# Optimization experiments

Hardware: AMD Instinct MI355X
Metric: run time of the kernel (lower is better)

## Reference

```python
import jax, jax.numpy as jnp
import numpy as np

STRIDE = 32
NUM_CLASSES = 20
CONF_THRESH = 0.01
NMS_THRESH = 0.5
INPUT_H, INPUT_W = 1024, 1024
EPS = 1e-28


def make_grid(h, w):
    hs, ws = h // STRIDE, w // STRIDE
    gy, gx = jnp.meshgrid(jnp.arange(hs), jnp.arange(ws), indexing='ij')
    # [1, hs*ws, 2] (x, y) cell coordinates
    return jnp.stack([gx, gy], axis=-1).reshape(1, hs * ws, 2).astype(jnp.float32)


def decode_boxes(txtytwth, grid):
    # txtytwth: [B, N, 4] -> [xmin, ymin, xmax, ymax] in pixels
    cxy = (jax.nn.sigmoid(txtytwth[..., :2]) + grid) * STRIDE
    wh = jnp.exp(txtytwth[..., 2:])
    return jnp.concatenate([cxy - wh * 0.5, cxy + wh * 0.5], axis=-1)


def pairwise_iou(boxes):
    # boxes: [N, 4]; faithful to source: area without +1, w/h clamped to 1e-28
    x1, y1, x2, y2 = boxes[:, 0], boxes[:, 1], boxes[:, 2], boxes[:, 3]
    areas = (x2 - x1) * (y2 - y1)
    xx1 = jnp.maximum(x1[:, None], x1[None, :])
    yy1 = jnp.maximum(y1[:, None], y1[None, :])
    xx2 = jnp.minimum(x2[:, None], x2[None, :])
    yy2 = jnp.minimum(y2[:, None], y2[None, :])
    w = jnp.maximum(EPS, xx2 - xx1)
    h = jnp.maximum(EPS, yy2 - yy1)
    inter = w * h
    return inter / (areas[:, None] + areas[None, :] - inter)


def nms_single(boxes, scores, valid):
    # greedy NMS, fixed-shape: returns keep mask [N] in original order
    n = boxes.shape[0]
    order = jnp.argsort(-scores)
    b = boxes[order]
    v = valid[order]
    iou = pairwise_iou(b)  # [N, N]
    idx = jnp.arange(n)

    def body(i, keep):
        sup = keep[i] & (iou[i] > NMS_THRESH) & (idx > i)
        return keep & jnp.logical_not(sup)

    keep_sorted = jax.lax.fori_loop(0, n, body, v)
    return jnp.zeros(n, dtype=bool).at[order].set(keep_sorted)


def setup_inputs() -> dict:
    key = jax.random.key(0)
    k1, k2, k3 = jax.random.split(key, 3)
    feat = jax.random.normal(k1, (64, 512, 32, 32), dtype=jnp.float32)
    w_pred = jax.random.normal(k2, (25, 512), dtype=jnp.float32) * 0.05
    b_pred = jax.random.normal(k3, (25,), dtype=jnp.float32) * 0.05
    return {"feat": feat, "w_pred": w_pred, "b_pred": b_pred}


def reference(feat, w_pred, b_pred):
    B, C, hs, ws = feat.shape
    N = hs * ws
    # 1x1 conv head: [B, 25, hs, ws] -> [B, N, 25]
    pred = jnp.einsum('bchw,oc->bhwo', feat, w_pred) + b_pred
    pred = pred.reshape(B, N, 1 + NUM_CLASSES + 4)

    conf = jax.nn.sigmoid(pred[..., :1])                      # [B, N, 1]
    cls = jax.nn.softmax(pred[..., 1:1 + NUM_CLASSES], -1)    # [B, N, 20]
    boxes = decode_boxes(pred[..., 1 + NUM_CLASSES:], make_grid(INPUT_H, INPUT_W))
    scale = jnp.array([INPUT_W, INPUT_H, INPUT_W, INPUT_H], jnp.float32)
    boxes = jnp.clip(boxes / scale, 0.0, 1.0)                 # [B, N, 4] in [0,1]

    scores_all = conf * cls                                   # [B, N, 20]
    cls_inds = jnp.argmax(scores_all, axis=-1)                # [B, N]
    scores = jnp.max(scores_all, axis=-1)                     # [B, N]
    valid = scores > CONF_THRESH

    # class-aware NMS via per-class coordinate offset (boxes in [0,1])
    off_boxes = boxes + cls_inds[..., None].astype(jnp.float32) * 2.0
    keep = jax.vmap(nms_single)(off_boxes, scores, valid)     # [B, N] bool
    return boxes, scores, cls_inds.astype(jnp.int32), keep
```

## Files before the change

### kernel.cpp

```cpp
#include <hip/hip_runtime.h>
#include <hip/hip_bf16.h>

typedef unsigned long long u64;
typedef unsigned int u32;
typedef __attribute__((ext_vector_type(4))) double f64x4;

#define NB   64
#define NPOS 1024
#define NOUT 25
#define NCLS 20
#define WROW 32
#define BIGCAP 256
#define ECAP   2048
#define TINY_TH (30.0f / 1024.0f)

#define OFF_W64   0
#define OFF_B64   131072
#define OFF_BIGC  131328
#define OFF_BIGL  131584
#define OFF_EDGC  197120
#define OFF_EDGL  197376

__global__ __launch_bounds__(256) void k_cvt(const float* __restrict__ w,
                                             const float* __restrict__ bias,
                                             double* __restrict__ wpad,
                                             double* __restrict__ b64,
                                             int* __restrict__ bigcnt,
                                             int* __restrict__ edgecnt)
{
    int idx = blockIdx.x * 256 + threadIdx.x;
    if (idx < 512 * WROW) {
        int c = idx >> 5, o = idx & 31;
        wpad[idx] = (o < NOUT) ? (double)w[o * 512 + c] : 0.0;
    }
    if (idx < NOUT) b64[idx] = (double)bias[idx];
    if (idx < NB) { bigcnt[idx] = 0; edgecnt[idx] = 0; }
}

__device__ __forceinline__ void epilogue(const double* __restrict__ acc,
                                         const double* __restrict__ b64,
                                         int b, int n,
                                         float* __restrict__ boxes_out,
                                         float* __restrict__ scores_out,
                                         float* __restrict__ cls_out,
                                         int* __restrict__ bigcnt,
                                         int* __restrict__ biglist)
{
    double p[NOUT];
#pragma unroll
    for (int o = 0; o < NOUT; ++o) p[o] = acc[o] + b64[o];

    double conf = 1.0 / (1.0 + exp(-p[0]));
    double m = p[1]; int ci = 0;
#pragma unroll
    for (int i = 2; i <= NCLS; ++i) {
        if (p[i] > m) { m = p[i]; ci = i - 1; }
    }
    double ssum = 0.0;
#pragma unroll
    for (int i = 0; i < NCLS; ++i) ssum += exp(p[1 + i] - m);
    double best = conf / ssum;

    int gx = n & 31, gy = n >> 5;
    double sx = 1.0 / (1.0 + exp(-p[21]));
    double sy = 1.0 / (1.0 + exp(-p[22]));
    double cx = (sx + (double)gx) * 32.0;
    double cy = (sy + (double)gy) * 32.0;
    double bw = exp(p[23]), bh = exp(p[24]);
    double x1 = (cx - bw * 0.5) * (1.0 / 1024.0);
    double y1 = (cy - bh * 0.5) * (1.0 / 1024.0);
    double x2 = (cx + bw * 0.5) * (1.0 / 1024.0);
    double y2 = (cy + bh * 0.5) * (1.0 / 1024.0);
    x1 = fmin(fmax(x1, 0.0), 1.0); y1 = fmin(fmax(y1, 0.0), 1.0);
    x2 = fmin(fmax(x2, 0.0), 1.0); y2 = fmin(fmax(y2, 0.0), 1.0);

    float fx1 = (float)x1, fy1 = (float)y1, fx2 = (float)x2, fy2 = (float)y2;
    int gi = b * NPOS + n;
    ((float4*)boxes_out)[gi] = make_float4(fx1, fy1, fx2, fy2);
    scores_out[gi] = (float)best;
    cls_out[gi]    = (float)ci;

    if (!((fx2 - fx1 < TINY_TH) && (fy2 - fy1 < TINY_TH))) {
        int s = atomicAdd(&bigcnt[b], 1);
        if (s < BIGCAP) biglist[b * BIGCAP + s] = n;
    }
}

__global__ __launch_bounds__(256, 4) void k_main(const float* __restrict__ feat,
                                                 const double* __restrict__ wpad_g,
                                                 const double* __restrict__ b64,
                                                 float* __restrict__ boxes_out,
                                                 float* __restrict__ scores_out,
                                                 float* __restrict__ cls_out,
                                                 int* __restrict__ bigcnt,
                                                 int* __restrict__ biglist)
{
    __shared__ __align__(16) char smem[32768];
    float*  AbF = (float*)smem;
    double* BbF = (double*)(smem + 16384);
    double (*pd)[33] = (double(*)[33])smem;

    const int b   = blockIdx.y;
    const int tid = threadIdx.x;
    const int l   = tid & 63;
    const int wv  = tid >> 6;
    const int pg  = wv >> 1;
    const int oh  = wv & 1;
    const int n0  = blockIdx.x * 64;

    double ca = ((l >> 4) == 0) ? (double)(l & 15) : 0.0;
    double cb = ((l >> 4) == 0) ? 1.0 : 0.0;
    f64x4 cd = {0.0, 0.0, 0.0, 0.0};
    cd = __builtin_amdgcn_mfma_f64_16x16x4f64(ca, cb, cd, 0, 0, 0);
    int rmap[4];
#pragma unroll
    for (int v = 0; v < 4; ++v) {
        int r = (int)(cd[v] + 0.5);
        rmap[v] = (r < 0) ? 0 : (r > 15 ? 15 : r);
    }

    const float* __restrict__ featb = feat + (size_t)b * 512 * NPOS + n0;

#define A_SRC(C0, IT) (((const float4*)(featb + (size_t)((C0) + wv*8 + (IT)*4 + (l>>4)) * NPOS)) + (l & 15))
#define B_SRC(C0, IT) (((const double2*)(wpad_g + (size_t)((C0) + wv*8 + (IT)*4 + (l>>4)) * WROW)) + (l & 15))
#define A_DST(BUF, IT) ((float4*)(AbF + (BUF)*2048 + (wv*8 + (IT)*4) * 64 + l*4))
#define B_DST(BUF, IT) ((double2*)(BbF + (BUF)*1024 + (wv*8 + (IT)*4) * 32 + l*2))

    f64x4 acc0 = {0.0, 0.0, 0.0, 0.0};
    f64x4 acc1 = {0.0, 0.0, 0.0, 0.0};

    float4  ra0 = *A_SRC(0, 0), ra1 = *A_SRC(0, 1);
    double2 rb0 = *B_SRC(0, 0), rb1 = *B_SRC(0, 1);
    *A_DST(0, 0) = ra0;  *A_DST(0, 1) = ra1;
    *B_DST(0, 0) = rb0;  *B_DST(0, 1) = rb1;
    __syncthreads();

#pragma unroll 1
    for (int t = 0; t < 16; ++t) {
        const int buf = t & 1;
        const bool more = (t + 1) < 16;
        const int c1 = (t + 1) * 32;
        if (more) {
            ra0 = *A_SRC(c1, 0);  ra1 = *A_SRC(c1, 1);
            rb0 = *B_SRC(c1, 0);  rb1 = *B_SRC(c1, 1);
        }
#pragma unroll
        for (int s = 0; s < 8; ++s) {
            const int rowA = buf*2048 + (4*s + (l >> 4)) * 64 + pg * 32 + (l & 15);
            const int rowB = buf*1024 + (4*s + (l >> 4)) * 32 + oh * 16 + (l & 15);
            double av0 = (double)AbF[rowA];
            double av1 = (double)AbF[rowA + 16];
            double bv  = BbF[rowB];
            acc0 = __builtin_amdgcn_mfma_f64_16x16x4f64(av0, bv, acc0, 0, 0, 0);
            acc1 = __builtin_amdgcn_mfma_f64_16x16x4f64(av1, bv, acc1, 0, 0, 0);
        }
        if (more) {
            *A_DST(buf ^ 1, 0) = ra0;  *A_DST(buf ^ 1, 1) = ra1;
            *B_DST(buf ^ 1, 0) = rb0;  *B_DST(buf ^ 1, 1) = rb1;
        }
        __syncthreads();
    }
#undef A_SRC
#undef B_SRC
#undef A_DST
#undef B_DST

#pragma unroll
    for (int v = 0; v < 4; ++v) {
        int r0 = pg * 32 + rmap[v];
        pd[r0][oh * 16 + (l & 15)]      = acc0[v];
        pd[r0 + 16][oh * 16 + (l & 15)] = acc1[v];
    }
    __syncthreads();

    if (tid < 64) {
        double acc[NOUT];
#pragma unroll
        for (int o = 0; o < NOUT; ++o) acc[o] = pd[tid][o];
        int n = n0 + tid;
        epilogue(acc, b64, b, n, boxes_out, scores_out, cls_out, bigcnt, biglist);
    }
}

__device__ __forceinline__ void pair_check(int b, int p, int i,
                                           float4 bp, float ap, int cp,
                                           const float4* __restrict__ boxes4,
                                           const float* __restrict__ scores,
                                           const float* __restrict__ cls,
                                           int* __restrict__ edgecnt,
                                           u32* __restrict__ edges,
                                           bool need_tiny_i)
{
    float si = scores[b * NPOS + i];
    if (si <= 0.01f) return;
    float4 bi = boxes4[b * NPOS + i];
    if (need_tiny_i) {
        if (!((bi.z - bi.x < TINY_TH) && (bi.w - bi.y < TINY_TH))) return;
    }
    if ((int)cls[b * NPOS + i] != cp) return;
    float xx1 = fmaxf(bi.x, bp.x), yy1 = fmaxf(bi.y, bp.y);
    float xx2 = fminf(bi.z, bp.z), yy2 = fminf(bi.w, bp.w);
    float ww = fmaxf(1e-28f, xx2 - xx1);
    float hh = fmaxf(1e-28f, yy2 - yy1);
    float inter = ww * hh;
    float ai = (bi.z - bi.x) * (bi.w - bi.y);
    float uni = ai + ap - inter;
    if (uni > 0.0f && inter > 0.5f * uni) {
        int u = p < i ? p : i, v = p < i ? i : p;
        int slot = atomicAdd(&edgecnt[b], 1);
        if (slot < ECAP) edges[(size_t)b * ECAP + slot] = ((u32)u << 16) | (u32)v;
    }
}

__global__ __launch_bounds__(256) void k_edge(const float4* __restrict__ boxes4,
                                              const float* __restrict__ scores,
                                              const float* __restrict__ cls,
                                              const int* __restrict__ bigcnt,
                                              const int* __restrict__ biglist,
                                              int* __restrict__ edgecnt,
                                              u32* __restrict__ edges)
{
    const int b = blockIdx.y;
    const int p = blockIdx.x * 256 + threadIdx.x;
    const float sp = scores[b * NPOS + p];
    if (sp <= 0.01f) return;
    const float4 bp = boxes4[b * NPOS + p];
    const float ap = (bp.z - bp.x) * (bp.w - bp.y);
    const int cp = (int)cls[b * NPOS + p];
    const bool tinyp = (bp.z - bp.x < TINY_TH) && (bp.w - bp.y < TINY_TH);
    const int gx = p & 31, gy = p >> 5;

    if (tinyp) {
        if (gy > 0 && gx > 0)  pair_check(b, p, p - 33, bp, ap, cp, boxes4, scores, cls, edgecnt, edges, true);
        if (gy > 0)            pair_check(b, p, p - 32, bp, ap, cp, boxes4, scores, cls, edgecnt, edges, true);
        if (gy > 0 && gx < 31) pair_check(b, p, p - 31, bp, ap, cp, boxes4, scores, cls, edgecnt, edges, true);
        if (gx > 0)            pair_check(b, p, p - 1,  bp, ap, cp, boxes4, scores, cls, edgecnt, edges, true);
    }
    int nb = bigcnt[b]; if (nb > BIGCAP) nb = BIGCAP;
    for (int t = 0; t < nb; ++t) {
        int q = biglist[b * BIGCAP + t];
        if (q == p) continue;
        if (!tinyp && p > q) continue;
        pair_check(b, p, q, bp, ap, cp, boxes4, scores, cls, edgecnt, edges, false);
    }
}

__global__ __launch_bounds__(64) void k_resolve(const float* __restrict__ scores,
                                                const int* __restrict__ edgecnt,
                                                const u32* __restrict__ edges,
                                                float* __restrict__ keep_out)
{
    __shared__ u64 keepw[16];
    __shared__ u64 done[ECAP / 64];
    const int b = blockIdx.x, lane = threadIdx.x;

    for (int t = 0; t < 16; ++t) {
        bool v = scores[b * NPOS + t * 64 + lane] > 0.01f;
        u64 w = __ballot(v);
        if (lane == 0) keepw[t] = w;
    }
    if (lane < ECAP / 64) done[lane] = 0ull;
    __syncthreads();

    int E = edgecnt[b]; if (E > ECAP) E = ECAP;
    if (lane == 0 && E > 0) {
        const u32* eb = edges + (size_t)b * ECAP;
        for (int it = 0; it < E; ++it) {
            int bestj = -1, bidx = 0, bsup = 0, btgt = 0;
            float bs = -1.0f;
            for (int j = 0; j < E; ++j) {
                if ((done[j >> 6] >> (j & 63)) & 1ull) continue;
                u32 e = eb[j];
                int u = (int)(e >> 16), v = (int)(e & 0xffffu);
                float su = scores[b * NPOS + u], sv = scores[b * NPOS + v];
                int sup, tgt; float ss;
                if (su > sv || (su == sv && u < v)) { sup = u; tgt = v; ss = su; }
                else                                { sup = v; tgt = u; ss = sv; }
                if (bestj < 0 || ss > bs || (ss == bs && sup < bidx)) {
                    bestj = j; bs = ss; bidx = sup; bsup = sup; btgt = tgt;
                }
            }
            done[bestj >> 6] |= 1ull << (bestj & 63);
            if ((keepw[bsup >> 6] >> (bsup & 63)) & 1ull)
                keepw[btgt >> 6] &= ~(1ull << (btgt & 63));
        }
    }
    __syncthreads();

    for (int t = 0; t < 16; ++t) {
        u64 w = keepw[t];
        keep_out[b * NPOS + t * 64 + lane] = ((w >> lane) & 1ull) ? 1.0f : 0.0f;
    }
}

extern "C" void kernel_launch(void* const* d_in, const int* in_sizes, int n_in,
                              void* d_out, int out_size, void* d_ws, size_t ws_size,
                              hipStream_t stream)
{
    const float* feat = (const float*)d_in[0];
    const float* w    = (const float*)d_in[1];
    const float* bias = (const float*)d_in[2];

    float* out = (float*)d_out;
    float* boxes_out  = out;
    float* scores_out = out + NB * NPOS * 4;
    float* cls_out    = out + NB * NPOS * 5;
    float* keep_out   = out + NB * NPOS * 6;

    char* ws = (char*)d_ws;
    double* wpad   = (double*)(ws + OFF_W64);
    double* b64    = (double*)(ws + OFF_B64);
    int*    bigcnt = (int*)   (ws + OFF_BIGC);
    int*    biglist= (int*)   (ws + OFF_BIGL);
    int*    edgecnt= (int*)   (ws + OFF_EDGC);
    u32*    edges  = (u32*)   (ws + OFF_EDGL);

    hipLaunchKernelGGL(k_cvt,    dim3(64),     dim3(256), 0, stream, w, bias, wpad,
                       b64, bigcnt, edgecnt);
    hipLaunchKernelGGL(k_main,   dim3(16, 64), dim3(256), 0, stream, feat, wpad, b64,
                       boxes_out, scores_out, cls_out, bigcnt, biglist);
    hipLaunchKernelGGL(k_edge,   dim3(4, 64),  dim3(256), 0, stream,
                       (const float4*)boxes_out, scores_out, cls_out,
                       bigcnt, biglist, edgecnt, edges);
    hipLaunchKernelGGL(k_resolve, dim3(64),    dim3(64),  0, stream, scores_out,
                       edgecnt, edges, keep_out);
}
```

Measured before the change: 70.44 us.

## Fuse edge build and NMS resolve into one per-batch kernel; async LDS loads

Merges the edge-finding and greedy-resolve kernels into one per-image block that keeps scores and the edge list in shared memory, removing a launch and global atomics and edge traffic. The GEMM staging loop also switches from register-staged copies to direct global-to-LDS async loads. Trade-offs: edge finding now runs on only 64 blocks instead of 256, and edge capacity drops to 1024, which could truncate edges in dense cases. The async copies are issued before a barrier with no explicit wait on their completion, so correctness relies on the barrier and compiler inserting the needed waits.

```diff
diff --git a/kernel.cpp b/kernel.cpp
--- a/kernel.cpp
+++ b/kernel.cpp
@@ -11,22 +11,19 @@
 #define NCLS 20
 #define WROW 32
 #define BIGCAP 256
-#define ECAP   2048
+#define ECAP_S 1024
 #define TINY_TH (30.0f / 1024.0f)
 
 #define OFF_W64   0
 #define OFF_B64   131072
 #define OFF_BIGC  131328
 #define OFF_BIGL  131584
-#define OFF_EDGC  197120
-#define OFF_EDGL  197376
 
 __global__ __launch_bounds__(256) void k_cvt(const float* __restrict__ w,
                                              const float* __restrict__ bias,
                                              double* __restrict__ wpad,
                                              double* __restrict__ b64,
-                                             int* __restrict__ bigcnt,
-                                             int* __restrict__ edgecnt)
+                                             int* __restrict__ bigcnt)
 {
     int idx = blockIdx.x * 256 + threadIdx.x;
     if (idx < 512 * WROW) {
@@ -34,7 +31,14 @@
         wpad[idx] = (o < NOUT) ? (double)w[o * 512 + c] : 0.0;
     }
     if (idx < NOUT) b64[idx] = (double)bias[idx];
-    if (idx < NB) { bigcnt[idx] = 0; edgecnt[idx] = 0; }
+    if (idx < NB) bigcnt[idx] = 0;
+}
+
+__device__ __forceinline__ void async_cp16(const void* g, void* l)
+{
+    __builtin_amdgcn_global_load_lds(
+        (const __attribute__((address_space(1))) u32*)g,
+        (__attribute__((address_space(3))) u32*)l, 16, 0, 0);
 }
 
 __device__ __forceinline__ void epilogue(const double* __restrict__ acc,
@@ -121,29 +125,27 @@
 
     const float* __restrict__ featb = feat + (size_t)b * 512 * NPOS + n0;
 
-#define A_SRC(C0, IT) (((const float4*)(featb + (size_t)((C0) + wv*8 + (IT)*4 + (l>>4)) * NPOS)) + (l & 15))
-#define B_SRC(C0, IT) (((const double2*)(wpad_g + (size_t)((C0) + wv*8 + (IT)*4 + (l>>4)) * WROW)) + (l & 15))
-#define A_DST(BUF, IT) ((float4*)(AbF + (BUF)*2048 + (wv*8 + (IT)*4) * 64 + l*4))
-#define B_DST(BUF, IT) ((double2*)(BbF + (BUF)*1024 + (wv*8 + (IT)*4) * 32 + l*2))
+#define A_G(C0, IT) (featb + (size_t)((C0) + wv*8 + (IT)*4 + (l>>4)) * NPOS + (l & 15)*4)
+#define B_G(C0, IT) (wpad_g + (size_t)((C0) + wv*8 + (IT)*4 + (l>>4)) * WROW + (l & 15)*2)
+#define A_L(BUF, IT) (AbF + (BUF)*2048 + (wv*8 + (IT)*4) * 64)
+#define B_L(BUF, IT) (BbF + (BUF)*1024 + (wv*8 + (IT)*4) * 32)
+#define ISSUE(C0, BUF) do {                               \
+    async_cp16(A_G(C0, 0), A_L(BUF, 0));                  \
+    async_cp16(A_G(C0, 1), A_L(BUF, 1));                  \
+    async_cp16(B_G(C0, 0), B_L(BUF, 0));                  \
+    async_cp16(B_G(C0, 1), B_L(BUF, 1));                  \
+} while (0)
 
     f64x4 acc0 = {0.0, 0.0, 0.0, 0.0};
     f64x4 acc1 = {0.0, 0.0, 0.0, 0.0};
 
-    float4  ra0 = *A_SRC(0, 0), ra1 = *A_SRC(0, 1);
-    double2 rb0 = *B_SRC(0, 0), rb1 = *B_SRC(0, 1);
-    *A_DST(0, 0) = ra0;  *A_DST(0, 1) = ra1;
-    *B_DST(0, 0) = rb0;  *B_DST(0, 1) = rb1;
+    ISSUE(0, 0);
     __syncthreads();
 
 #pragma unroll 1
     for (int t = 0; t < 16; ++t) {
         const int buf = t & 1;
-        const bool more = (t + 1) < 16;
-        const int c1 = (t + 1) * 32;
-        if (more) {
-            ra0 = *A_SRC(c1, 0);  ra1 = *A_SRC(c1, 1);
-            rb0 = *B_SRC(c1, 0);  rb1 = *B_SRC(c1, 1);
-        }
+        if (t + 1 < 16) ISSUE((t + 1) * 32, buf ^ 1);
 #pragma unroll
         for (int s = 0; s < 8; ++s) {
             const int rowA = buf*2048 + (4*s + (l >> 4)) * 64 + pg * 32 + (l & 15);
@@ -154,16 +156,13 @@
             acc0 = __builtin_amdgcn_mfma_f64_16x16x4f64(av0, bv, acc0, 0, 0, 0);
             acc1 = __builtin_amdgcn_mfma_f64_16x16x4f64(av1, bv, acc1, 0, 0, 0);
         }
-        if (more) {
-            *A_DST(buf ^ 1, 0) = ra0;  *A_DST(buf ^ 1, 1) = ra1;
-            *B_DST(buf ^ 1, 0) = rb0;  *B_DST(buf ^ 1, 1) = rb1;
-        }
         __syncthreads();
     }
-#undef A_SRC
-#undef B_SRC
-#undef A_DST
-#undef B_DST
+#undef A_G
+#undef B_G
+#undef A_L
+#undef B_L
+#undef ISSUE
 
 #pragma unroll
     for (int v = 0; v < 4; ++v) {
@@ -182,97 +181,94 @@
     }
 }
 
-__device__ __forceinline__ void pair_check(int b, int p, int i,
-                                           float4 bp, float ap, int cp,
-                                           const float4* __restrict__ boxes4,
-                                           const float* __restrict__ scores,
-                                           const float* __restrict__ cls,
-                                           int* __restrict__ edgecnt,
-                                           u32* __restrict__ edges,
-                                           bool need_tiny_i)
-{
-    float si = scores[b * NPOS + i];
-    if (si <= 0.01f) return;
-    float4 bi = boxes4[b * NPOS + i];
-    if (need_tiny_i) {
-        if (!((bi.z - bi.x < TINY_TH) && (bi.w - bi.y < TINY_TH))) return;
-    }
-    if ((int)cls[b * NPOS + i] != cp) return;
-    float xx1 = fmaxf(bi.x, bp.x), yy1 = fmaxf(bi.y, bp.y);
-    float xx2 = fminf(bi.z, bp.z), yy2 = fminf(bi.w, bp.w);
-    float ww = fmaxf(1e-28f, xx2 - xx1);
-    float hh = fmaxf(1e-28f, yy2 - yy1);
-    float inter = ww * hh;
-    float ai = (bi.z - bi.x) * (bi.w - bi.y);
-    float uni = ai + ap - inter;
-    if (uni > 0.0f && inter > 0.5f * uni) {
-        int u = p < i ? p : i, v = p < i ? i : p;
-        int slot = atomicAdd(&edgecnt[b], 1);
-        if (slot < ECAP) edges[(size_t)b * ECAP + slot] = ((u32)u << 16) | (u32)v;
-    }
-}
-
-__global__ __launch_bounds__(256) void k_edge(const float4* __restrict__ boxes4,
-                                              const float* __restrict__ scores,
-                                              const float* __restrict__ cls,
-                                              const int* __restrict__ bigcnt,
-                                              const int* __restrict__ biglist,
-                                              int* __restrict__ edgecnt,
-                                              u32* __restrict__ edges)
-{
-    const int b = blockIdx.y;
-    const int p = blockIdx.x * 256 + threadIdx.x;
-    const float sp = scores[b * NPOS + p];
-    if (sp <= 0.01f) return;
-    const float4 bp = boxes4[b * NPOS + p];
-    const float ap = (bp.z - bp.x) * (bp.w - bp.y);
-    const int cp = (int)cls[b * NPOS + p];
-    const bool tinyp = (bp.z - bp.x < TINY_TH) && (bp.w - bp.y < TINY_TH);
-    const int gx = p & 31, gy = p >> 5;
-
-    if (tinyp) {
-        if (gy > 0 && gx > 0)  pair_check(b, p, p - 33, bp, ap, cp, boxes4, scores, cls, edgecnt, edges, true);
-        if (gy > 0)            pair_check(b, p, p - 32, bp, ap, cp, boxes4, scores, cls, edgecnt, edges, true);
-        if (gy > 0 && gx < 31) pair_check(b, p, p - 31, bp, ap, cp, boxes4, scores, cls, edgecnt, edges, true);
-        if (gx > 0)            pair_check(b, p, p - 1,  bp, ap, cp, boxes4, scores, cls, edgecnt, edges, true);
-    }
+__global__ __launch_bounds__(256) void k_nms(const float4* __restrict__ boxes4,
+                                             const float* __restrict__ scores,
+                                             const float* __restrict__ cls,
+                                             const int* __restrict__ bigcnt,
+                                             const int* __restrict__ biglist,
+                                             float* __restrict__ keep_out)
+{
+    __shared__ float sc[NPOS];
+    __shared__ u32 eds[ECAP_S];
+    __shared__ int ecnt;
+    __shared__ u64 keepw[16];
+    __shared__ u64 done[ECAP_S / 64];
+    const int b = blockIdx.x, tid = threadIdx.x;
+    const int lane = tid & 63, w4 = tid >> 6;
+
+    if (tid == 0) ecnt = 0;
+    if (tid < ECAP_S / 64) done[tid] = 0ull;
+#pragma unroll
+    for (int t = 0; t < 4; ++t) {
+        int word = w4 * 4 + t;
+        float s = scores[b * NPOS + word * 64 + lane];
+        sc[word * 64 + lane] = s;
+        u64 vb = __ballot(s > 0.01f);
+        if (lane == 0) keepw[word] = vb;
+    }
+    __syncthreads();
+
     int nb = bigcnt[b]; if (nb > BIGCAP) nb = BIGCAP;
-    for (int t = 0; t < nb; ++t) {
-        int q = biglist[b * BIGCAP + t];
-        if (q == p) continue;
-        if (!tinyp && p > q) continue;
-        pair_check(b, p, q, bp, ap, cp, boxes4, scores, cls, edgecnt, edges, false);
-    }
-}
-
-__global__ __launch_bounds__(64) void k_resolve(const float* __restrict__ scores,
-                                                const int* __restrict__ edgecnt,
-                                                const u32* __restrict__ edges,
-                                                float* __restrict__ keep_out)
-{
-    __shared__ u64 keepw[16];
-    __shared__ u64 done[ECAP / 64];
-    const int b = blockIdx.x, lane = threadIdx.x;
-
-    for (int t = 0; t < 16; ++t) {
-        bool v = scores[b * NPOS + t * 64 + lane] > 0.01f;
-        u64 w = __ballot(v);
-        if (lane == 0) keepw[t] = w;
-    }
-    if (lane < ECAP / 64) done[lane] = 0ull;
-    __syncthreads();
-
-    int E = edgecnt[b]; if (E > ECAP) E = ECAP;
-    if (lane == 0 && E > 0) {
-        const u32* eb = edges + (size_t)b * ECAP;
+#pragma unroll 1
+    for (int p = tid; p < NPOS; p += 256) {
+        float sp = sc[p];
+        if (sp <= 0.01f) continue;
+        float4 bp = boxes4[b * NPOS + p];
+        float ap = (bp.z - bp.x) * (bp.w - bp.y);
+        int cp = (int)cls[b * NPOS + p];
+        bool tinyp = (bp.z - bp.x < TINY_TH) && (bp.w - bp.y < TINY_TH);
+        int gx = p & 31, gy = p >> 5;
+
+#define PAIR(I, NEEDTINY) do {                                                \
+    int i_ = (I);                                                             \
+    if (sc[i_] > 0.01f) {                                                     \
+        float4 bi = boxes4[b * NPOS + i_];                                    \
+        bool ok = true;                                                       \
+        if (NEEDTINY)                                                         \
+            ok = (bi.z - bi.x < TINY_TH) && (bi.w - bi.y < TINY_TH);          \
+        if (ok && (int)cls[b * NPOS + i_] == cp) {                            \
+            float xx1 = fmaxf(bi.x, bp.x), yy1 = fmaxf(bi.y, bp.y);           \
+            float xx2 = fminf(bi.z, bp.z), yy2 = fminf(bi.w, bp.w);           \
+            float ww = fmaxf(1e-28f, xx2 - xx1);                              \
+            float hh = fmaxf(1e-28f, yy2 - yy1);                              \
+            float inter = ww * hh;                                            \
+            float ai = (bi.z - bi.x) * (bi.w - bi.y);                         \
+            float uni = ai + ap - inter;                                      \
+            if (uni > 0.0f && inter > 0.5f * uni) {                           \
+                int u_ = p < i_ ? p : i_, v_ = p < i_ ? i_ : p;               \
+                int slot = atomicAdd(&ecnt, 1);                               \
+                if (slot < ECAP_S) eds[slot] = ((u32)u_ << 16) | (u32)v_;     \
+            }                                                                 \
+        }                                                                     \
+    }                                                                         \
+} while (0)
+
+        if (tinyp) {
+            if (gy > 0 && gx > 0)  PAIR(p - 33, true);
+            if (gy > 0)            PAIR(p - 32, true);
+            if (gy > 0 && gx < 31) PAIR(p - 31, true);
+            if (gx > 0)            PAIR(p - 1,  true);
+        }
+        for (int t2 = 0; t2 < nb; ++t2) {
+            int q = biglist[b * BIGCAP + t2];
+            if (q == p) continue;
+            if (!tinyp && p > q) continue;
+            PAIR(q, false);
+        }
+#undef PAIR
+    }
+    __syncthreads();
+
+    if (tid == 0) {
+        int E = ecnt; if (E > ECAP_S) E = ECAP_S;
         for (int it = 0; it < E; ++it) {
             int bestj = -1, bidx = 0, bsup = 0, btgt = 0;
             float bs = -1.0f;
             for (int j = 0; j < E; ++j) {
                 if ((done[j >> 6] >> (j & 63)) & 1ull) continue;
-                u32 e = eb[j];
+                u32 e = eds[j];
                 int u = (int)(e >> 16), v = (int)(e & 0xffffu);
-                float su = scores[b * NPOS + u], sv = scores[b * NPOS + v];
+                float su = sc[u], sv = sc[v];
                 int sup, tgt; float ss;
                 if (su > sv || (su == sv && u < v)) { sup = u; tgt = v; ss = su; }
                 else                                { sup = v; tgt = u; ss = sv; }
@@ -287,9 +283,11 @@
     }
     __syncthreads();
 
-    for (int t = 0; t < 16; ++t) {
-        u64 w = keepw[t];
-        keep_out[b * NPOS + t * 64 + lane] = ((w >> lane) & 1ull) ? 1.0f : 0.0f;
+#pragma unroll
+    for (int t = 0; t < 4; ++t) {
+        int word = w4 * 4 + t;
+        u64 kw = keepw[word];
+        keep_out[b * NPOS + word * 64 + lane] = ((kw >> lane) & 1ull) ? 1.0f : 0.0f;
     }
 }
 
@@ -312,16 +310,12 @@
     double* b64    = (double*)(ws + OFF_B64);
     int*    bigcnt = (int*)   (ws + OFF_BIGC);
     int*    biglist= (int*)   (ws + OFF_BIGL);
-    int*    edgecnt= (int*)   (ws + OFF_EDGC);
-    u32*    edges  = (u32*)   (ws + OFF_EDGL);
-
-    hipLaunchKernelGGL(k_cvt,    dim3(64),     dim3(256), 0, stream, w, bias, wpad,
-                       b64, bigcnt, edgecnt);
-    hipLaunchKernelGGL(k_main,   dim3(16, 64), dim3(256), 0, stream, feat, wpad, b64,
+
+    hipLaunchKernelGGL(k_cvt,  dim3(64),     dim3(256), 0, stream, w, bias, wpad,
+                       b64, bigcnt);
+    hipLaunchKernelGGL(k_main, dim3(16, 64), dim3(256), 0, stream, feat, wpad, b64,
                        boxes_out, scores_out, cls_out, bigcnt, biglist);
-    hipLaunchKernelGGL(k_edge,   dim3(4, 64),  dim3(256), 0, stream,
+    hipLaunchKernelGGL(k_nms,  dim3(64),     dim3(256), 0, stream,
                        (const float4*)boxes_out, scores_out, cls_out,
-                       bigcnt, biglist, edgecnt, edges);
-    hipLaunchKernelGGL(k_resolve, dim3(64),    dim3(64),  0, stream, scores_out,
-                       edgecnt, edges, keep_out);
-}
+                       bigcnt, biglist, keep_out);
+}
```

After: 73.11 us. +3.8%, slower.
